# Kernel tuning notes

Measured on AMD Instinct MI355X. Metric: run time of the kernel, lower is better.

The kernel has to match this reference:

```python
import jax, jax.numpy as jnp
import numpy as np

L_MAX = 3
C = 512  # channels per degree


def _triples(l_max):
    ts = []
    for l1 in range(l_max + 1):
        for l2 in range(l1, l_max + 1):
            for L in range(l2 - l1, min(l_max, l1 + l2) + 1):
                ts.append((l1, l2, L))
    return ts


def setup_inputs() -> dict:
    key = jax.random.key(0)
    keys = jax.random.split(key, 4 + len(_triples(L_MAX)))
    inp = {}
    ki = 0
    for l in range(L_MAX + 1):
        inp[f"x{l}"] = jax.random.normal(keys[ki], (C, 2 * l + 1), dtype=jnp.float32)
        ki += 1
    for (l1, l2, L) in _triples(L_MAX):
        # cg[L, l2, l1] has shape [2L+1, 2l2+1, 2l1+1]
        inp[f"cg_{L}_{l2}_{l1}"] = 0.1 * jax.random.normal(
            keys[ki], (2 * L + 1, 2 * l2 + 1, 2 * l1 + 1), dtype=jnp.float32)
        ki += 1
    return inp


def reference(x0, x1, x2, x3,
              cg_0_0_0, cg_1_1_0, cg_2_2_0, cg_3_3_0,
              cg_0_1_1, cg_1_1_1, cg_2_1_1, cg_1_2_1, cg_2_2_1, cg_3_2_1,
              cg_2_3_1, cg_3_3_1,
              cg_0_2_2, cg_1_2_2, cg_2_2_2, cg_3_2_2, cg_1_3_2, cg_2_3_2,
              cg_3_3_2,
              cg_0_3_3, cg_1_3_3, cg_2_3_3, cg_3_3_3):
    xs = [x0, x1, x2, x3]
    cg_list = [cg_0_0_0, cg_1_1_0, cg_2_2_0, cg_3_3_0,
               cg_0_1_1, cg_1_1_1, cg_2_1_1, cg_1_2_1, cg_2_2_1, cg_3_2_1,
               cg_2_3_1, cg_3_3_1,
               cg_0_2_2, cg_1_2_2, cg_2_2_2, cg_3_2_2, cg_1_3_2, cg_2_3_2,
               cg_3_3_2,
               cg_0_3_3, cg_1_3_3, cg_2_3_3, cg_3_3_3]
    cg = dict(zip(_triples(L_MAX), cg_list))
    out = {L: [] for L in range(L_MAX + 1)}
    for (l1, l2, L) in _triples(L_MAX):
        # product: [i, j, 2L+1]
        p = jnp.einsum('Mnm,im,jn->ijM', cg[(l1, l2, L)], xs[l1], xs[l2])
        out[L].append(p.reshape(-1, 2 * L + 1))
    return tuple(jnp.concatenate(out[L], axis=0) for L in range(L_MAX + 1))
```

## Files before the change

kernel.cpp:

```cpp
#include <hip/hip_runtime.h>


#define C2 (512 * 512)

struct Ptrs {
    const float* x[4];
    const float* cg[23];
};

#define TRIPLE_LIST(F) \
    F(0, 0, 0, 0, 0, 0, 0) \
    F(1, 0, 1, 1, 4, 1, 0) \
    F(2, 0, 2, 2, 22, 4, 1) \
    F(3, 0, 3, 3, 57, 9, 0) \
    F(4, 1, 1, 0, 1, 16, 0) \
    F(5, 1, 1, 1, 7, 19, 1) \
    F(6, 1, 1, 2, 27, 22, 1) \
    F(7, 1, 2, 1, 10, 25, 1) \
    F(8, 1, 2, 2, 32, 30, 1) \
    F(9, 1, 2, 3, 64, 35, 0) \
    F(10, 1, 3, 2, 37, 40, 1) \
    F(11, 1, 3, 3, 71, 47, 0) \
    F(12, 2, 2, 0, 2, 54, 0) \
    F(13, 2, 2, 1, 13, 59, 1) \
    F(14, 2, 2, 2, 42, 64, 1) \
    F(15, 2, 2, 3, 78, 69, 0) \
    F(16, 2, 3, 1, 16, 74, 1) \
    F(17, 2, 3, 2, 47, 81, 1) \
    F(18, 2, 3, 3, 85, 88, 0) \
    F(19, 3, 3, 0, 3, 95, 0) \
    F(20, 3, 3, 1, 19, 102, 1) \
    F(21, 3, 3, 2, 52, 109, 1) \
    F(22, 3, 3, 3, 92, 116, 0)

#define XBASE(L2) ((L2) == 0 ? 0 : ((L2) == 1 ? 1 : ((L2) == 2 ? 4 : 9)))

__global__ __launch_bounds__(256) void cg_tp_kernel(Ptrs p, float* __restrict__ out) {
    __shared__ float ysh[123 * 8];

    const int tid = threadIdx.x;
    const int b = blockIdx.x;
    const int i = b >> 2;
    const int jh = (b >> 1) & 1;
    const int half = b & 1;
    const int j = (jh << 8) + tid;

    if (tid < 123) {
        const int r = tid;
#define YC(T, L1, L2, LL, OB, RB, HF)                                          \
        if (r >= (RB) && r < (RB) + (2 * L2 + 1)) {                            \
            const int n = r - (RB);                                            \
            const float* cg = p.cg[T];                                         \
            const float* xi = p.x[L1] + i * (2 * L1 + 1);                      \
            _Pragma("unroll")                                                  \
            for (int M = 0; M < 2 * LL + 1; ++M) {                             \
                float s = 0.f;                                                 \
                _Pragma("unroll")                                              \
                for (int m = 0; m < 2 * L1 + 1; ++m)                           \
                    s = fmaf(cg[(M * (2 * L2 + 1) + n) * (2 * L1 + 1) + m],    \
                             xi[m], s);                                        \
                ysh[r * 8 + M] = s;                                            \
            }                                                                  \
        }
        TRIPLE_LIST(YC)
#undef YC
    }

    float xj[16];
    {
        xj[0] = p.x[0][j];
        const float* x1 = p.x[1] + j * 3;
        #pragma unroll
        for (int m = 0; m < 3; ++m) xj[1 + m] = x1[m];
        const float* x2 = p.x[2] + j * 5;
        #pragma unroll
        for (int m = 0; m < 5; ++m) xj[4 + m] = x2[m];
        const float* x3 = p.x[3] + j * 7;
        #pragma unroll
        for (int m = 0; m < 7; ++m) xj[9 + m] = x3[m];
    }

    __syncthreads();

    const int pair = i * 512 + j;

#define TC(T, L1, L2, LL, OB, RB, HF)                                          \
    if (half == (HF)) {                                                        \
        constexpr int NW = 2 * LL + 1;                                         \
        float acc[NW] = {};                                                    \
        const float* y = ysh + (RB) * 8;                                       \
        _Pragma("unroll")                                                      \
        for (int n = 0; n < 2 * L2 + 1; ++n) {                                 \
            const float xv = xj[XBASE(L2) + n];                                \
            _Pragma("unroll")                                                  \
            for (int M = 0; M < NW; ++M)                                       \
                acc[M] = fmaf(y[n * 8 + M], xv, acc[M]);                       \
        }                                                                      \
        float* o = out + (size_t)(OB) * C2 + (size_t)pair * NW;                \
        _Pragma("unroll")                                                      \
        for (int M = 0; M < NW; ++M) o[M] = acc[M];                            \
    }
    TRIPLE_LIST(TC)
#undef TC
}

extern "C" void kernel_launch(void* const* d_in, const int* in_sizes, int n_in,
                              void* d_out, int out_size, void* d_ws, size_t ws_size,
                              hipStream_t stream) {
    Ptrs p;
    for (int l = 0; l < 4; ++l) p.x[l] = (const float*)d_in[l];
    for (int t = 0; t < 23; ++t) p.cg[t] = (const float*)d_in[4 + t];
    cg_tp_kernel<<<dim3(2048), dim3(256), 0, stream>>>(p, (float*)d_out);
}
```

Baseline: 176.5 us.

## Precompute per-i CG-contracted rows in separate kernel and stream outputs nontemporally

Moves the per-i contraction of CG coefficients with x[l1] into a separate y_kernel that writes a 123x8 table per i to workspace, and the main kernel then loads it with float4 copies. It also merges the two half-blocks so each block computes all 23 triples for its pairs, which halves the grid and removes the duplicated y computation. Output stores become nontemporal to avoid polluting cache with the large write stream. This costs an extra kernel launch plus a workspace round trip, and gives each thread more work and more register pressure.

```diff
diff --git a/kernel.cpp b/kernel.cpp
--- a/kernel.cpp
+++ b/kernel.cpp
@@ -2,6 +2,8 @@
 
 
 #define C2 (512 * 512)
+#define YROWS 123
+#define YSTRIDE (YROWS * 8)
 
 struct Ptrs {
     const float* x[4];
@@ -9,61 +11,91 @@
 };
 
 #define TRIPLE_LIST(F) \
-    F(0, 0, 0, 0, 0, 0, 0) \
-    F(1, 0, 1, 1, 4, 1, 0) \
-    F(2, 0, 2, 2, 22, 4, 1) \
-    F(3, 0, 3, 3, 57, 9, 0) \
-    F(4, 1, 1, 0, 1, 16, 0) \
-    F(5, 1, 1, 1, 7, 19, 1) \
-    F(6, 1, 1, 2, 27, 22, 1) \
-    F(7, 1, 2, 1, 10, 25, 1) \
-    F(8, 1, 2, 2, 32, 30, 1) \
-    F(9, 1, 2, 3, 64, 35, 0) \
-    F(10, 1, 3, 2, 37, 40, 1) \
-    F(11, 1, 3, 3, 71, 47, 0) \
-    F(12, 2, 2, 0, 2, 54, 0) \
-    F(13, 2, 2, 1, 13, 59, 1) \
-    F(14, 2, 2, 2, 42, 64, 1) \
-    F(15, 2, 2, 3, 78, 69, 0) \
-    F(16, 2, 3, 1, 16, 74, 1) \
-    F(17, 2, 3, 2, 47, 81, 1) \
-    F(18, 2, 3, 3, 85, 88, 0) \
-    F(19, 3, 3, 0, 3, 95, 0) \
-    F(20, 3, 3, 1, 19, 102, 1) \
-    F(21, 3, 3, 2, 52, 109, 1) \
-    F(22, 3, 3, 3, 92, 116, 0)
+    F(0, 0, 0, 0, 0, 0) \
+    F(1, 0, 1, 1, 4, 1) \
+    F(2, 0, 2, 2, 22, 4) \
+    F(3, 0, 3, 3, 57, 9) \
+    F(4, 1, 1, 0, 1, 16) \
+    F(5, 1, 1, 1, 7, 19) \
+    F(6, 1, 1, 2, 27, 22) \
+    F(7, 1, 2, 1, 10, 25) \
+    F(8, 1, 2, 2, 32, 30) \
+    F(9, 1, 2, 3, 64, 35) \
+    F(10, 1, 3, 2, 37, 40) \
+    F(11, 1, 3, 3, 71, 47) \
+    F(12, 2, 2, 0, 2, 54) \
+    F(13, 2, 2, 1, 13, 59) \
+    F(14, 2, 2, 2, 42, 64) \
+    F(15, 2, 2, 3, 78, 69) \
+    F(16, 2, 3, 1, 16, 74) \
+    F(17, 2, 3, 2, 47, 81) \
+    F(18, 2, 3, 3, 85, 88) \
+    F(19, 3, 3, 0, 3, 95) \
+    F(20, 3, 3, 1, 19, 102) \
+    F(21, 3, 3, 2, 52, 109) \
+    F(22, 3, 3, 3, 92, 116)
 
 #define XBASE(L2) ((L2) == 0 ? 0 : ((L2) == 1 ? 1 : ((L2) == 2 ? 4 : 9)))
 
-__global__ __launch_bounds__(256) void cg_tp_kernel(Ptrs p, float* __restrict__ out) {
-    __shared__ float ysh[123 * 8];
+__global__ __launch_bounds__(128) void y_kernel(Ptrs p, float* __restrict__ yall) {
+    const int i = blockIdx.x;
+    const int r = threadIdx.x;
+    if (r >= YROWS) return;
+    float* yrow = yall + (size_t)i * YSTRIDE + r * 8;
+#define YC(T, L1, L2, LL, OB, RB)                                              \
+    if (r >= (RB) && r < (RB) + (2 * L2 + 1)) {                                \
+        const int n = r - (RB);                                                \
+        const float* cg = p.cg[T];                                             \
+        const float* xi = p.x[L1] + i * (2 * L1 + 1);                          \
+        _Pragma("unroll")                                                      \
+        for (int M = 0; M < 2 * LL + 1; ++M) {                                 \
+            float s = 0.f;                                                     \
+            _Pragma("unroll")                                                  \
+            for (int m = 0; m < 2 * L1 + 1; ++m)                               \
+                s = fmaf(cg[(M * (2 * L2 + 1) + n) * (2 * L1 + 1) + m],        \
+                         xi[m], s);                                            \
+            yrow[M] = s;                                                       \
+        }                                                                      \
+    }
+    TRIPLE_LIST(YC)
+#undef YC
+}
+
+template <bool USE_WS>
+__global__ __launch_bounds__(256) void cg_tp_kernel(Ptrs p,
+                                                    const float* __restrict__ yall,
+                                                    float* __restrict__ out) {
+    __shared__ float ysh[YSTRIDE];
 
     const int tid = threadIdx.x;
     const int b = blockIdx.x;
-    const int i = b >> 2;
-    const int jh = (b >> 1) & 1;
-    const int half = b & 1;
-    const int j = (jh << 8) + tid;
+    const int i = b >> 1;
+    const int j = ((b & 1) << 8) + tid;
 
-    if (tid < 123) {
-        const int r = tid;
-#define YC(T, L1, L2, LL, OB, RB, HF)                                          \
-        if (r >= (RB) && r < (RB) + (2 * L2 + 1)) {                            \
-            const int n = r - (RB);                                            \
-            const float* cg = p.cg[T];                                         \
-            const float* xi = p.x[L1] + i * (2 * L1 + 1);                      \
-            _Pragma("unroll")                                                  \
-            for (int M = 0; M < 2 * LL + 1; ++M) {                             \
-                float s = 0.f;                                                 \
+    if (USE_WS) {
+        if (tid < 246)
+            ((float4*)ysh)[tid] = ((const float4*)(yall + (size_t)i * YSTRIDE))[tid];
+    } else {
+        if (tid < YROWS) {
+            const int r = tid;
+#define YC(T, L1, L2, LL, OB, RB)                                              \
+            if (r >= (RB) && r < (RB) + (2 * L2 + 1)) {                        \
+                const int n = r - (RB);                                        \
+                const float* cg = p.cg[T];                                     \
+                const float* xi = p.x[L1] + i * (2 * L1 + 1);                  \
                 _Pragma("unroll")                                              \
-                for (int m = 0; m < 2 * L1 + 1; ++m)                           \
-                    s = fmaf(cg[(M * (2 * L2 + 1) + n) * (2 * L1 + 1) + m],    \
-                             xi[m], s);                                        \
-                ysh[r * 8 + M] = s;                                            \
-            }                                                                  \
+                for (int M = 0; M < 2 * LL + 1; ++M) {                         \
+                    float s = 0.f;                                             \
+                    _Pragma("unroll")                                          \
+                    for (int m = 0; m < 2 * L1 + 1; ++m)                       \
+                        s = fmaf(cg[(M * (2 * L2 + 1) + n) * (2 * L1 + 1) + m],\
+                                 xi[m], s);                                    \
+                    ysh[r * 8 + M] = s;                                        \
+                }                                                              \
+            }
+            TRIPLE_LIST(YC)
+#undef YC
         }
-        TRIPLE_LIST(YC)
-#undef YC
     }
 
     float xj[16];
@@ -84,8 +116,8 @@
 
     const int pair = i * 512 + j;
 
-#define TC(T, L1, L2, LL, OB, RB, HF)                                          \
-    if (half == (HF)) {                                                        \
+#define TC(T, L1, L2, LL, OB, RB)                                              \
+    {                                                                          \
         constexpr int NW = 2 * LL + 1;                                         \
         float acc[NW] = {};                                                    \
         const float* y = ysh + (RB) * 8;                                       \
@@ -98,7 +130,7 @@
         }                                                                      \
         float* o = out + (size_t)(OB) * C2 + (size_t)pair * NW;                \
         _Pragma("unroll")                                                      \
-        for (int M = 0; M < NW; ++M) o[M] = acc[M];                            \
+        for (int M = 0; M < NW; ++M) __builtin_nontemporal_store(acc[M], o + M); \
     }
     TRIPLE_LIST(TC)
 #undef TC
@@ -110,5 +142,13 @@
     Ptrs p;
     for (int l = 0; l < 4; ++l) p.x[l] = (const float*)d_in[l];
     for (int t = 0; t < 23; ++t) p.cg[t] = (const float*)d_in[4 + t];
-    cg_tp_kernel<<<dim3(2048), dim3(256), 0, stream>>>(p, (float*)d_out);
+
+    const size_t y_bytes = (size_t)512 * YSTRIDE * sizeof(float);
+    if (ws_size >= y_bytes) {
+        float* yall = (float*)d_ws;
+        y_kernel<<<dim3(512), dim3(128), 0, stream>>>(p, yall);
+        cg_tp_kernel<true><<<dim3(1024), dim3(256), 0, stream>>>(p, yall, (float*)d_out);
+    } else {
+        cg_tp_kernel<false><<<dim3(1024), dim3(256), 0, stream>>>(p, nullptr, (float*)d_out);
+    }
 }
```

Result: slower. 212.0 us (+20.1%).
